# Performance work log

Measured on AMD Instinct MI355X. Metric: run time of the kernel, lower is better.

## Reference

```python
import jax, jax.numpy as jnp
import numpy as np
from jax import lax

# LNS semantics: values are held as (sign, log_base|x|); exact conversion round-trips
# make log-domain mul/add mathematically identical to float conv/linear/relu, so the
# faithful reference is the equivalent float pipeline.

def _conv(x, w, b):
    # x: [B,C,H,W], w: [O,C,kh,kw] (torch layout), stride 1, no padding
    y = lax.conv_general_dilated(x, w, window_strides=(1, 1), padding='VALID',
                                 dimension_numbers=('NCHW', 'OIHW', 'NCHW'))
    return y + b[None, :, None, None]

def _maxpool2(x):
    return lax.reduce_window(x, -jnp.inf, lax.max,
                             window_dimensions=(1, 1, 2, 2),
                             window_strides=(1, 1, 2, 2), padding='VALID')

def setup_inputs() -> dict:
    key = jax.random.key(0)
    ks = jax.random.split(key, 9)
    s = lambda k, shape, fan: jax.random.normal(k, shape, jnp.float32) * (1.0 / np.sqrt(fan))
    return {
        'x': jax.random.normal(ks[0], (512, 1, 54, 54), jnp.float32),
        'conv1_w': s(ks[1], (32, 1, 3, 3), 9),
        'conv1_b': s(ks[2], (32,), 9),
        'conv2_w': s(ks[3], (64, 32, 3, 3), 32 * 9),
        'conv2_b': s(ks[4], (64,), 32 * 9),
        'fc1_w': s(ks[5], (128, 9216), 9216),
        'fc1_b': s(ks[6], (128,), 9216),
        'fc2_w': s(ks[7], (10, 128), 128),
        'fc2_b': s(ks[8], (10,), 128),
    }

def reference(x, conv1_w, conv1_b, conv2_w, conv2_b, fc1_w, fc1_b, fc2_w, fc2_b):
    h = jnp.maximum(_conv(x, conv1_w, conv1_b), 0.0)          # [B,32,52,52]
    h = _maxpool2(h)                                          # [B,32,26,26]
    h = jnp.maximum(_conv(h, conv2_w, conv2_b), 0.0)          # [B,64,24,24]
    h = _maxpool2(h)                                          # [B,64,12,12]
    h = h.reshape(h.shape[0], -1)                             # [B,9216]
    h = jnp.maximum(h @ fc1_w.T + fc1_b, 0.0)                 # [B,128]
    return h @ fc2_w.T + fc2_b                                # [B,10]
```

## Files before the change

### kernel.cpp

```cpp
#include <hip/hip_runtime.h>


#define B 512
#define POS 676
#define ICP 36
#define P2SZ (64*12*12)

typedef unsigned short ushort_t;
typedef ushort_t ushort4v __attribute__((ext_vector_type(4)));
typedef short s16x8 __attribute__((ext_vector_type(8)));
typedef float f32x4 __attribute__((ext_vector_type(4)));
typedef float f32x2 __attribute__((ext_vector_type(2)));

__device__ __forceinline__ ushort_t f2bf(float f) {
    union { float f; unsigned u; } a; a.f = f;
    unsigned r = a.u + 0x7FFFu + ((a.u >> 16) & 1u);
    return (ushort_t)(r >> 16);
}
__device__ __forceinline__ float bf2f(ushort_t u) {
    union { unsigned u; float f; } a; a.u = ((unsigned)u) << 16;
    return a.f;
}

#define N_WR (64 * 9 * 32)
#define N_WF (128 * 9216)
#define CONV1_BLOCKS 1664
#define PREP_BLOCKS  4680

__global__ __launch_bounds__(256) void conv1_prep(const float* __restrict__ x,
                                                  const float* __restrict__ w,
                                                  const float* __restrict__ bias,
                                                  const float* __restrict__ c2w,
                                                  const float* __restrict__ f1w,
                                                  ushort_t* __restrict__ out,
                                                  ushort_t* __restrict__ wr,
                                                  ushort_t* __restrict__ wfb) {
    int blk = blockIdx.x;
    if (blk >= CONV1_BLOCKS) {
        int t = (blk - CONV1_BLOCKS) * 256 + threadIdx.x;
        if (t < N_WR) {
            int ic  = t & 31;
            int tap = (t >> 5) % 9;
            int oc  = t / 288;
            wr[t] = f2bf(c2w[oc * 288 + ic * 9 + tap]);
        } else if (t < N_WR + N_WF) {
            int i = t - N_WR;
            wfb[i] = f2bf(f1w[i]);
        }
        return;
    }
    int t = blk * 256 + threadIdx.x;
    int ic = t & 31;
    int r  = t >> 5;
    int py = r % 26;
    int b  = r / 26;

    const float* wp = w + ic * 9;
    float w00 = wp[0], w01 = wp[1], w02 = wp[2];
    float w10 = wp[3], w11 = wp[4], w12 = wp[5];
    float w20 = wp[6], w21 = wp[7], w22 = wp[8];
    float bv = bias[ic];

    const float* xr = x + b * (54 * 54) + (2 * py) * 54;
    ushort_t* po = out + ((size_t)b * POS + py * 26) * 32 + ic;

    f32x2 p[4], q[4];
#pragma unroll
    for (int rr = 0; rr < 4; ++rr) p[rr] = *reinterpret_cast<const f32x2*>(xr + rr * 54);
#pragma unroll
    for (int rr = 0; rr < 4; ++rr) q[rr] = *reinterpret_cast<const f32x2*>(xr + rr * 54 + 2);

#pragma unroll
    for (int px = 0; px < 26; ++px) {
        f32x2 mid[4];
#pragma unroll
        for (int rr = 0; rr < 4; ++rr) mid[rr] = (f32x2){p[rr].y, q[rr].x};

        f32x2 s0 = p[0] * (f32x2)w00 + mid[0] * (f32x2)w01 + q[0] * (f32x2)w02
                 + p[1] * (f32x2)w10 + mid[1] * (f32x2)w11 + q[1] * (f32x2)w12
                 + p[2] * (f32x2)w20 + mid[2] * (f32x2)w21 + q[2] * (f32x2)w22;
        f32x2 s1 = p[1] * (f32x2)w00 + mid[1] * (f32x2)w01 + q[1] * (f32x2)w02
                 + p[2] * (f32x2)w10 + mid[2] * (f32x2)w11 + q[2] * (f32x2)w12
                 + p[3] * (f32x2)w20 + mid[3] * (f32x2)w21 + q[3] * (f32x2)w22;

        float m = fmaxf(fmaxf(s0.x, s0.y), fmaxf(s1.x, s1.y));
        po[px * 32] = f2bf(fmaxf(m + bv, 0.0f));
        if (px < 25) {
#pragma unroll
            for (int rr = 0; rr < 4; ++rr) {
                p[rr] = q[rr];
                q[rr] = *reinterpret_cast<const f32x2*>(xr + rr * 54 + 2 * px + 4);
            }
        }
    }
}

__global__ __launch_bounds__(256) void conv2_mfma(const ushort_t* __restrict__ p1,
                                                  const ushort_t* __restrict__ wr,
                                                  const float* __restrict__ bias,
                                                  ushort_t* __restrict__ pool2) {
    __shared__ ushort_t lds[260 * ICP];
    int blk = blockIdx.x;
    int b = blk / 3, c = blk % 3;
    int tid = threadIdx.x;

    const ushort_t* src = p1 + ((size_t)b * POS + 8 * c * 26) * 32;
    for (int t = tid; t < 260 * 8; t += 256) {
        int pos = t >> 3, off = (t & 7) * 4;
        ushort4v v = *reinterpret_cast<const ushort4v*>(src + pos * 32 + off);
        *reinterpret_cast<ushort4v*>(&lds[pos * ICP + off]) = v;
    }
    __syncthreads();

    int lane = tid & 63, wid = tid >> 6;
    int quad = lane >> 4, lr = lane & 15;

    int ebase[3];
#pragma unroll
    for (int t = 0; t < 3; ++t) {
        int m  = t * 16 + lr;
        int yl = m / 24;
        int xx = m - yl * 24;
        ebase[t] = ((2 * wid + yl) * 26 + xx) * ICP + quad * 8;
    }

    f32x4 acc[3][4];
#pragma unroll
    for (int t = 0; t < 3; ++t)
#pragma unroll
        for (int n = 0; n < 4; ++n) acc[t][n] = (f32x4){0.f, 0.f, 0.f, 0.f};

    const ushort_t* wb = wr + (size_t)lr * 288 + quad * 8;

#pragma unroll
    for (int tap = 0; tap < 9; ++tap) {
        int ky = tap / 3, kx = tap % 3;
        int koff = (ky * 26 + kx) * ICP;
        s16x8 a[3];
#pragma unroll
        for (int t = 0; t < 3; ++t) {
            union { ushort4v s[2]; s16x8 v; } u;
            u.s[0] = *reinterpret_cast<const ushort4v*>(&lds[ebase[t] + koff]);
            u.s[1] = *reinterpret_cast<const ushort4v*>(&lds[ebase[t] + koff + 4]);
            a[t] = u.v;
        }
        s16x8 bf[4];
#pragma unroll
        for (int n = 0; n < 4; ++n)
            bf[n] = *reinterpret_cast<const s16x8*>(wb + n * 4608 + tap * 32);
#pragma unroll
        for (int t = 0; t < 3; ++t)
#pragma unroll
            for (int n = 0; n < 4; ++n)
                acc[t][n] = __builtin_amdgcn_mfma_f32_16x16x32_bf16(a[t], bf[n], acc[t][n], 0, 0, 0);
    }
    __syncthreads();

    ushort_t* scr = lds + wid * 1536;
#pragma unroll
    for (int t = 0; t < 3; ++t)
#pragma unroll
        for (int n = 0; n < 4; ++n) {
            int oc = n * 16 + lr;
            int i0 = t * 8 + quad * 2;
            float v0 = fmaxf(acc[t][n][0], acc[t][n][1]);
            float v1 = fmaxf(acc[t][n][2], acc[t][n][3]);
            union { ushort_t u2[2]; unsigned w; } pk;
            pk.u2[0] = f2bf(v0); pk.u2[1] = f2bf(v1);
            *reinterpret_cast<unsigned*>(&scr[oc * 24 + i0]) = pk.w;
        }
    int oc = lane;
    const ushort_t* row = scr + oc * 24;
    float bv = bias[oc];
    int py = c * 4 + wid;
    ushort_t outv[12];
#pragma unroll
    for (int px = 0; px < 12; ++px) {
        float r0 = bf2f(row[px]);
        float r1 = bf2f(row[px + 12]);
        outv[px] = f2bf(fmaxf(fmaxf(r0, r1) + bv, 0.0f));
    }
    ushort_t* po = pool2 + ((size_t)(b * 64 + oc) * 144 + py * 12);
#pragma unroll
    for (int q = 0; q < 3; ++q)
        *reinterpret_cast<ushort4v*>(po + q * 4) =
            (ushort4v){outv[q*4+0], outv[q*4+1], outv[q*4+2], outv[q*4+3]};
}

__global__ __launch_bounds__(256) void fc1_mfma(const ushort_t* __restrict__ A,
                                                 const ushort_t* __restrict__ W,
                                                 float* __restrict__ Cpart) {
    int tid = threadIdx.x;
    int lane = tid & 63, wid = tid >> 6;
    int lr = lane & 15, quad = lane >> 4;
    int w  = blockIdx.x * 4 + wid;
    int nt = w & 3;
    int ks = (w >> 2) & 31;
    int mt = w >> 7;

    int m0 = mt * 32;
    int n0 = nt * 32;
    int k0 = ks * 288 + quad * 8;
    const ushort_t* a0 = A + (size_t)(m0 + lr) * 9216 + k0;
    const ushort_t* a1 = a0 + (size_t)16 * 9216;
    const ushort_t* b0 = W + (size_t)(n0 + lr) * 9216 + k0;
    const ushort_t* b1 = b0 + (size_t)16 * 9216;

    f32x4 acc[2][2];
#pragma unroll
    for (int i = 0; i < 2; ++i)
#pragma unroll
        for (int j = 0; j < 2; ++j) acc[i][j] = (f32x4){0.f, 0.f, 0.f, 0.f};

#pragma unroll
    for (int kk = 0; kk < 9; ++kk) {
        s16x8 av0 = *reinterpret_cast<const s16x8*>(a0 + kk * 32);
        s16x8 av1 = *reinterpret_cast<const s16x8*>(a1 + kk * 32);
        s16x8 bv0 = *reinterpret_cast<const s16x8*>(b0 + kk * 32);
        s16x8 bv1 = *reinterpret_cast<const s16x8*>(b1 + kk * 32);
        acc[0][0] = __builtin_amdgcn_mfma_f32_16x16x32_bf16(av0, bv0, acc[0][0], 0, 0, 0);
        acc[0][1] = __builtin_amdgcn_mfma_f32_16x16x32_bf16(av0, bv1, acc[0][1], 0, 0, 0);
        acc[1][0] = __builtin_amdgcn_mfma_f32_16x16x32_bf16(av1, bv0, acc[1][0], 0, 0, 0);
        acc[1][1] = __builtin_amdgcn_mfma_f32_16x16x32_bf16(av1, bv1, acc[1][1], 0, 0, 0);
    }

    float* cp = Cpart + (size_t)ks * (512 * 128);
#pragma unroll
    for (int i = 0; i < 2; ++i) {
        int crow = m0 + i * 16 + quad * 4;
#pragma unroll
        for (int j = 0; j < 2; ++j) {
            int col = n0 + j * 16 + lr;
#pragma unroll
            for (int r = 0; r < 4; ++r)
                cp[(size_t)(crow + r) * 128 + col] = acc[i][j][r];
        }
    }
}

__global__ __launch_bounds__(128) void fc1fc2(const float* __restrict__ Cpart,
                                              const float* __restrict__ b1,
                                              const float* __restrict__ w2,
                                              const float* __restrict__ b2,
                                              float* __restrict__ out) {
    __shared__ float h[128];
    int b = blockIdx.x, k = threadIdx.x;
    float s = 0.f;
#pragma unroll
    for (int ks = 0; ks < 32; ++ks) s += Cpart[(size_t)ks * (512 * 128) + b * 128 + k];
    h[k] = fmaxf(s + b1[k], 0.0f);
    __syncthreads();
    if (k < 10) {
        const float* wp = w2 + k * 128;
        float acc = 0.f;
#pragma unroll 8
        for (int j = 0; j < 128; ++j) acc += h[j] * wp[j];
        out[b * 10 + k] = acc + b2[k];
    }
}

extern "C" void kernel_launch(void* const* d_in, const int* in_sizes, int n_in,
                              void* d_out, int out_size, void* d_ws, size_t ws_size,
                              hipStream_t stream) {
    const float* x       = (const float*)d_in[0];
    const float* conv1_w = (const float*)d_in[1];
    const float* conv1_b = (const float*)d_in[2];
    const float* conv2_w = (const float*)d_in[3];
    const float* conv2_b = (const float*)d_in[4];
    const float* fc1_w   = (const float*)d_in[5];
    const float* fc1_b   = (const float*)d_in[6];
    const float* fc2_w   = (const float*)d_in[7];
    const float* fc2_b   = (const float*)d_in[8];
    float* out = (float*)d_out;

    char* ws = (char*)d_ws;
    ushort_t* pool1 = (ushort_t*)ws;
    ws += (size_t)B * POS * 32 * sizeof(ushort_t);
    ushort_t* wr = (ushort_t*)ws;
    ws += N_WR * sizeof(ushort_t) + 128;
    ushort_t* wfb = (ushort_t*)ws;
    ws += N_WF * sizeof(ushort_t) + 128;
    ushort_t* pool2b = (ushort_t*)ws;
    ws += (size_t)B * P2SZ * sizeof(ushort_t) + 128;
    float* Cpart = (float*)ws;
    ws += (size_t)32 * 512 * 128 * sizeof(float) + 128;

    {
        conv1_prep<<<CONV1_BLOCKS + PREP_BLOCKS, 256, 0, stream>>>(
            x, conv1_w, conv1_b, conv2_w, fc1_w, pool1, wr, wfb);
    }
    {
        conv2_mfma<<<B * 3, 256, 0, stream>>>(pool1, wr, conv2_b, pool2b);
    }
    {
        fc1_mfma<<<512, 256, 0, stream>>>(pool2b, wfb, Cpart);
    }
    {
        fc1fc2<<<B, 128, 0, stream>>>(Cpart, fc1_b, fc2_w, fc2_b, out);
    }
}
```

Measured before the change: 131.3 us.

## Fuse conv2, fc1 and fc2 into one persistent kernel with grid barriers

Merges the conv2, fc1 split-K and fc1-reduce/fc2 kernels into a single launch of 768 blocks. Each block handles two conv2 chunks, then software grid barriers built on atomic counters separate the stages. The barrier counters are reset inside the conv1 prep kernel. This removes two kernel launch gaps and their tail effects. In exchange it relies on all 768 blocks being co-resident (256 CUs at 3 blocks each), otherwise it deadlocks, and it adds atomic spin-wait costs.

New measurement: 437.7 us. 233% more time.

```diff
diff --git a/kernel.cpp b/kernel.cpp
--- a/kernel.cpp
+++ b/kernel.cpp
@@ -26,6 +26,7 @@
 #define N_WF (128 * 9216)
 #define CONV1_BLOCKS 1664
 #define PREP_BLOCKS  4680
+#define FUSED_BLOCKS 768
 
 __global__ __launch_bounds__(256) void conv1_prep(const float* __restrict__ x,
                                                   const float* __restrict__ w,
@@ -34,9 +35,11 @@
                                                   const float* __restrict__ f1w,
                                                   ushort_t* __restrict__ out,
                                                   ushort_t* __restrict__ wr,
-                                                  ushort_t* __restrict__ wfb) {
+                                                  ushort_t* __restrict__ wfb,
+                                                  unsigned* __restrict__ barrier_ctr) {
     int blk = blockIdx.x;
     if (blk >= CONV1_BLOCKS) {
+        if (blk == CONV1_BLOCKS && threadIdx.x < 2) barrier_ctr[threadIdx.x] = 0;
         int t = (blk - CONV1_BLOCKS) * 256 + threadIdx.x;
         if (t < N_WR) {
             int ic  = t & 31;
@@ -95,167 +98,188 @@
     }
 }
 
-__global__ __launch_bounds__(256) void conv2_mfma(const ushort_t* __restrict__ p1,
-                                                  const ushort_t* __restrict__ wr,
-                                                  const float* __restrict__ bias,
-                                                  ushort_t* __restrict__ pool2) {
+__device__ __forceinline__ void grid_barrier(unsigned* ctr, unsigned target) {
+    __threadfence();
+    __syncthreads();
+    if (threadIdx.x == 0) {
+        atomicAdd(ctr, 1u);
+        while (__hip_atomic_load(ctr, __ATOMIC_RELAXED, __HIP_MEMORY_SCOPE_AGENT) < target)
+            __builtin_amdgcn_s_sleep(8);
+        __threadfence();
+    }
+    __syncthreads();
+}
+
+__global__ __launch_bounds__(256, 3) void fused_net(const ushort_t* __restrict__ p1,
+                                                    const ushort_t* __restrict__ wr,
+                                                    const float* __restrict__ c2b,
+                                                    const ushort_t* __restrict__ wfb,
+                                                    const float* __restrict__ b1,
+                                                    const float* __restrict__ w2,
+                                                    const float* __restrict__ b2,
+                                                    ushort_t* __restrict__ pool2,
+                                                    float* __restrict__ Cpart,
+                                                    float* __restrict__ out,
+                                                    unsigned* __restrict__ barrier_ctr) {
     __shared__ ushort_t lds[260 * ICP];
     int blk = blockIdx.x;
-    int b = blk / 3, c = blk % 3;
     int tid = threadIdx.x;
-
-    const ushort_t* src = p1 + ((size_t)b * POS + 8 * c * 26) * 32;
-    for (int t = tid; t < 260 * 8; t += 256) {
-        int pos = t >> 3, off = (t & 7) * 4;
-        ushort4v v = *reinterpret_cast<const ushort4v*>(src + pos * 32 + off);
-        *reinterpret_cast<ushort4v*>(&lds[pos * ICP + off]) = v;
-    }
-    __syncthreads();
-
     int lane = tid & 63, wid = tid >> 6;
     int quad = lane >> 4, lr = lane & 15;
 
-    int ebase[3];
-#pragma unroll
-    for (int t = 0; t < 3; ++t) {
-        int m  = t * 16 + lr;
-        int yl = m / 24;
-        int xx = m - yl * 24;
-        ebase[t] = ((2 * wid + yl) * 26 + xx) * ICP + quad * 8;
-    }
-
-    f32x4 acc[3][4];
-#pragma unroll
-    for (int t = 0; t < 3; ++t)
-#pragma unroll
-        for (int n = 0; n < 4; ++n) acc[t][n] = (f32x4){0.f, 0.f, 0.f, 0.f};
-
-    const ushort_t* wb = wr + (size_t)lr * 288 + quad * 8;
-
-#pragma unroll
-    for (int tap = 0; tap < 9; ++tap) {
-        int ky = tap / 3, kx = tap % 3;
-        int koff = (ky * 26 + kx) * ICP;
-        s16x8 a[3];
+#pragma unroll 1
+    for (int cc = 0; cc < 2; ++cc) {
+        int ch = blk * 2 + cc;
+        int b = ch / 3, c = ch % 3;
+
+        const ushort_t* src = p1 + ((size_t)b * POS + 8 * c * 26) * 32;
+        for (int t = tid; t < 260 * 8; t += 256) {
+            int pos = t >> 3, off = (t & 7) * 4;
+            ushort4v v = *reinterpret_cast<const ushort4v*>(src + pos * 32 + off);
+            *reinterpret_cast<ushort4v*>(&lds[pos * ICP + off]) = v;
+        }
+        __syncthreads();
+
+        int ebase[3];
 #pragma unroll
         for (int t = 0; t < 3; ++t) {
-            union { ushort4v s[2]; s16x8 v; } u;
-            u.s[0] = *reinterpret_cast<const ushort4v*>(&lds[ebase[t] + koff]);
-            u.s[1] = *reinterpret_cast<const ushort4v*>(&lds[ebase[t] + koff + 4]);
-            a[t] = u.v;
-        }
-        s16x8 bf[4];
-#pragma unroll
-        for (int n = 0; n < 4; ++n)
-            bf[n] = *reinterpret_cast<const s16x8*>(wb + n * 4608 + tap * 32);
+            int m  = t * 16 + lr;
+            int yl = m / 24;
+            int xx = m - yl * 24;
+            ebase[t] = ((2 * wid + yl) * 26 + xx) * ICP + quad * 8;
+        }
+
+        f32x4 acc[3][4];
 #pragma unroll
         for (int t = 0; t < 3; ++t)
 #pragma unroll
+            for (int n = 0; n < 4; ++n) acc[t][n] = (f32x4){0.f, 0.f, 0.f, 0.f};
+
+        const ushort_t* wb = wr + (size_t)lr * 288 + quad * 8;
+
+#pragma unroll
+        for (int tap = 0; tap < 9; ++tap) {
+            int ky = tap / 3, kx = tap % 3;
+            int koff = (ky * 26 + kx) * ICP;
+            s16x8 a[3];
+#pragma unroll
+            for (int t = 0; t < 3; ++t) {
+                union { ushort4v s[2]; s16x8 v; } u;
+                u.s[0] = *reinterpret_cast<const ushort4v*>(&lds[ebase[t] + koff]);
+                u.s[1] = *reinterpret_cast<const ushort4v*>(&lds[ebase[t] + koff + 4]);
+                a[t] = u.v;
+            }
+            s16x8 bf[4];
+#pragma unroll
             for (int n = 0; n < 4; ++n)
-                acc[t][n] = __builtin_amdgcn_mfma_f32_16x16x32_bf16(a[t], bf[n], acc[t][n], 0, 0, 0);
-    }
-    __syncthreads();
-
-    ushort_t* scr = lds + wid * 1536;
-#pragma unroll
-    for (int t = 0; t < 3; ++t)
-#pragma unroll
-        for (int n = 0; n < 4; ++n) {
-            int oc = n * 16 + lr;
-            int i0 = t * 8 + quad * 2;
-            float v0 = fmaxf(acc[t][n][0], acc[t][n][1]);
-            float v1 = fmaxf(acc[t][n][2], acc[t][n][3]);
-            union { ushort_t u2[2]; unsigned w; } pk;
-            pk.u2[0] = f2bf(v0); pk.u2[1] = f2bf(v1);
-            *reinterpret_cast<unsigned*>(&scr[oc * 24 + i0]) = pk.w;
-        }
-    int oc = lane;
-    const ushort_t* row = scr + oc * 24;
-    float bv = bias[oc];
-    int py = c * 4 + wid;
-    ushort_t outv[12];
-#pragma unroll
-    for (int px = 0; px < 12; ++px) {
-        float r0 = bf2f(row[px]);
-        float r1 = bf2f(row[px + 12]);
-        outv[px] = f2bf(fmaxf(fmaxf(r0, r1) + bv, 0.0f));
-    }
-    ushort_t* po = pool2 + ((size_t)(b * 64 + oc) * 144 + py * 12);
-#pragma unroll
-    for (int q = 0; q < 3; ++q)
-        *reinterpret_cast<ushort4v*>(po + q * 4) =
-            (ushort4v){outv[q*4+0], outv[q*4+1], outv[q*4+2], outv[q*4+3]};
-}
-
-__global__ __launch_bounds__(256) void fc1_mfma(const ushort_t* __restrict__ A,
-                                                 const ushort_t* __restrict__ W,
-                                                 float* __restrict__ Cpart) {
-    int tid = threadIdx.x;
-    int lane = tid & 63, wid = tid >> 6;
-    int lr = lane & 15, quad = lane >> 4;
-    int w  = blockIdx.x * 4 + wid;
-    int nt = w & 3;
-    int ks = (w >> 2) & 31;
-    int mt = w >> 7;
-
-    int m0 = mt * 32;
-    int n0 = nt * 32;
-    int k0 = ks * 288 + quad * 8;
-    const ushort_t* a0 = A + (size_t)(m0 + lr) * 9216 + k0;
-    const ushort_t* a1 = a0 + (size_t)16 * 9216;
-    const ushort_t* b0 = W + (size_t)(n0 + lr) * 9216 + k0;
-    const ushort_t* b1 = b0 + (size_t)16 * 9216;
-
-    f32x4 acc[2][2];
-#pragma unroll
-    for (int i = 0; i < 2; ++i)
-#pragma unroll
-        for (int j = 0; j < 2; ++j) acc[i][j] = (f32x4){0.f, 0.f, 0.f, 0.f};
-
-#pragma unroll
-    for (int kk = 0; kk < 9; ++kk) {
-        s16x8 av0 = *reinterpret_cast<const s16x8*>(a0 + kk * 32);
-        s16x8 av1 = *reinterpret_cast<const s16x8*>(a1 + kk * 32);
-        s16x8 bv0 = *reinterpret_cast<const s16x8*>(b0 + kk * 32);
-        s16x8 bv1 = *reinterpret_cast<const s16x8*>(b1 + kk * 32);
-        acc[0][0] = __builtin_amdgcn_mfma_f32_16x16x32_bf16(av0, bv0, acc[0][0], 0, 0, 0);
-        acc[0][1] = __builtin_amdgcn_mfma_f32_16x16x32_bf16(av0, bv1, acc[0][1], 0, 0, 0);
-        acc[1][0] = __builtin_amdgcn_mfma_f32_16x16x32_bf16(av1, bv0, acc[1][0], 0, 0, 0);
-        acc[1][1] = __builtin_amdgcn_mfma_f32_16x16x32_bf16(av1, bv1, acc[1][1], 0, 0, 0);
-    }
-
-    float* cp = Cpart + (size_t)ks * (512 * 128);
-#pragma unroll
-    for (int i = 0; i < 2; ++i) {
-        int crow = m0 + i * 16 + quad * 4;
-#pragma unroll
-        for (int j = 0; j < 2; ++j) {
-            int col = n0 + j * 16 + lr;
-#pragma unroll
-            for (int r = 0; r < 4; ++r)
-                cp[(size_t)(crow + r) * 128 + col] = acc[i][j][r];
-        }
-    }
-}
-
-__global__ __launch_bounds__(128) void fc1fc2(const float* __restrict__ Cpart,
-                                              const float* __restrict__ b1,
-                                              const float* __restrict__ w2,
-                                              const float* __restrict__ b2,
-                                              float* __restrict__ out) {
-    __shared__ float h[128];
-    int b = blockIdx.x, k = threadIdx.x;
-    float s = 0.f;
-#pragma unroll
-    for (int ks = 0; ks < 32; ++ks) s += Cpart[(size_t)ks * (512 * 128) + b * 128 + k];
-    h[k] = fmaxf(s + b1[k], 0.0f);
-    __syncthreads();
-    if (k < 10) {
-        const float* wp = w2 + k * 128;
-        float acc = 0.f;
+                bf[n] = *reinterpret_cast<const s16x8*>(wb + n * 4608 + tap * 32);
+#pragma unroll
+            for (int t = 0; t < 3; ++t)
+#pragma unroll
+                for (int n = 0; n < 4; ++n)
+                    acc[t][n] = __builtin_amdgcn_mfma_f32_16x16x32_bf16(a[t], bf[n], acc[t][n], 0, 0, 0);
+        }
+        __syncthreads();
+
+        ushort_t* scr = lds + wid * 1536;
+#pragma unroll
+        for (int t = 0; t < 3; ++t)
+#pragma unroll
+            for (int n = 0; n < 4; ++n) {
+                int oc = n * 16 + lr;
+                int i0 = t * 8 + quad * 2;
+                float v0 = fmaxf(acc[t][n][0], acc[t][n][1]);
+                float v1 = fmaxf(acc[t][n][2], acc[t][n][3]);
+                union { ushort_t u2[2]; unsigned w; } pk;
+                pk.u2[0] = f2bf(v0); pk.u2[1] = f2bf(v1);
+                *reinterpret_cast<unsigned*>(&scr[oc * 24 + i0]) = pk.w;
+            }
+        int oc = lane;
+        const ushort_t* row = scr + oc * 24;
+        float bv = c2b[oc];
+        int py = c * 4 + wid;
+        ushort_t outv[12];
+#pragma unroll
+        for (int px = 0; px < 12; ++px) {
+            float r0 = bf2f(row[px]);
+            float r1 = bf2f(row[px + 12]);
+            outv[px] = f2bf(fmaxf(fmaxf(r0, r1) + bv, 0.0f));
+        }
+        ushort_t* po = pool2 + ((size_t)(b * 64 + oc) * 144 + py * 12);
+#pragma unroll
+        for (int q = 0; q < 3; ++q)
+            *reinterpret_cast<ushort4v*>(po + q * 4) =
+                (ushort4v){outv[q*4+0], outv[q*4+1], outv[q*4+2], outv[q*4+3]};
+        __syncthreads();
+    }
+
+    grid_barrier(&barrier_ctr[0], FUSED_BLOCKS);
+
+    if (blk < 512) {
+        int job = blk * 4 + wid;
+        int nt = job & 3;
+        int ks = (job >> 2) & 31;
+        int mt = job >> 7;
+
+        int m0 = mt * 32;
+        int n0 = nt * 32;
+        int k0 = ks * 288 + quad * 8;
+        const ushort_t* a0 = pool2 + (size_t)(m0 + lr) * 9216 + k0;
+        const ushort_t* a1 = a0 + (size_t)16 * 9216;
+        const ushort_t* b0 = wfb + (size_t)(n0 + lr) * 9216 + k0;
+        const ushort_t* bq1 = b0 + (size_t)16 * 9216;
+
+        f32x4 facc[2][2];
+#pragma unroll
+        for (int i = 0; i < 2; ++i)
+#pragma unroll
+            for (int j = 0; j < 2; ++j) facc[i][j] = (f32x4){0.f, 0.f, 0.f, 0.f};
+
+#pragma unroll
+        for (int kk = 0; kk < 9; ++kk) {
+            s16x8 av0 = *reinterpret_cast<const s16x8*>(a0 + kk * 32);
+            s16x8 av1 = *reinterpret_cast<const s16x8*>(a1 + kk * 32);
+            s16x8 bv0 = *reinterpret_cast<const s16x8*>(b0 + kk * 32);
+            s16x8 bv1 = *reinterpret_cast<const s16x8*>(bq1 + kk * 32);
+            facc[0][0] = __builtin_amdgcn_mfma_f32_16x16x32_bf16(av0, bv0, facc[0][0], 0, 0, 0);
+            facc[0][1] = __builtin_amdgcn_mfma_f32_16x16x32_bf16(av0, bv1, facc[0][1], 0, 0, 0);
+            facc[1][0] = __builtin_amdgcn_mfma_f32_16x16x32_bf16(av1, bv0, facc[1][0], 0, 0, 0);
+            facc[1][1] = __builtin_amdgcn_mfma_f32_16x16x32_bf16(av1, bv1, facc[1][1], 0, 0, 0);
+        }
+
+        float* cp = Cpart + (size_t)ks * (512 * 128);
+#pragma unroll
+        for (int i = 0; i < 2; ++i) {
+            int crow = m0 + i * 16 + quad * 4;
+#pragma unroll
+            for (int j = 0; j < 2; ++j) {
+                int col = n0 + j * 16 + lr;
+#pragma unroll
+                for (int r = 0; r < 4; ++r)
+                    cp[(size_t)(crow + r) * 128 + col] = facc[i][j][r];
+            }
+        }
+    }
+
+    grid_barrier(&barrier_ctr[1], FUSED_BLOCKS);
+
+    if (blk < 512) {
+        float* hsh = reinterpret_cast<float*>(lds);
+        int b = blk, k = tid;
+        if (k < 128) {
+            float s = 0.f;
+#pragma unroll
+            for (int ks = 0; ks < 32; ++ks) s += Cpart[(size_t)ks * (512 * 128) + b * 128 + k];
+            hsh[k] = fmaxf(s + b1[k], 0.0f);
+        }
+        __syncthreads();
+        if (k < 10) {
+            const float* wp = w2 + k * 128;
+            float acc = 0.f;
 #pragma unroll 8
-        for (int j = 0; j < 128; ++j) acc += h[j] * wp[j];
-        out[b * 10 + k] = acc + b2[k];
+            for (int j = 0; j < 128; ++j) acc += hsh[j] * wp[j];
+            out[b * 10 + k] = acc + b2[k];
+        }
     }
 }
 
@@ -284,18 +308,15 @@
     ws += (size_t)B * P2SZ * sizeof(ushort_t) + 128;
     float* Cpart = (float*)ws;
     ws += (size_t)32 * 512 * 128 * sizeof(float) + 128;
+    unsigned* barrier_ctr = (unsigned*)ws;
+    ws += 256;
 
     {
         conv1_prep<<<CONV1_BLOCKS + PREP_BLOCKS, 256, 0, stream>>>(
-            x, conv1_w, conv1_b, conv2_w, fc1_w, pool1, wr, wfb);
+            x, conv1_w, conv1_b, conv2_w, fc1_w, pool1, wr, wfb, barrier_ctr);
     }
     {
-        conv2_mfma<<<B * 3, 256, 0, stream>>>(pool1, wr, conv2_b, pool2b);
-    }
-    {
-        fc1_mfma<<<512, 256, 0, stream>>>(pool2b, wfb, Cpart);
-    }
-    {
-        fc1fc2<<<B, 128, 0, stream>>>(Cpart, fc1_b, fc2_w, fc2_b, out);
-    }
-}
+        fused_net<<<FUSED_BLOCKS, 256, 0, stream>>>(
+            pool1, wr, conv2_b, wfb, fc1_b, fc2_w, fc2_b, pool2b, Cpart, out, barrier_ctr);
+    }
+}
```

## Store pool2 channels-last with permuted fc1 weights and split conv1 rows

Applied to the files above, without the earlier changes.

Conv2 now writes its pooled output channels-last ([b][pos][oc]), and the fc1 weight conversion permutes columns to match, so the flatten order stays consistent. Conv1 work is split so each thread handles half a pooled row, doubling block count for more parallelism. Per-lane conv2 stores become contiguous across lanes (64 oc adjacent) instead of strided per-channel vectors, trading vectorized 8-byte stores for coalesced 2-byte stores. The weight permutation uses strided gathers from fc1_w, which may slow the prep step.

Result: no change. 131.2 us (-0.1%).

```diff
diff --git a/kernel.cpp b/kernel.cpp
--- a/kernel.cpp
+++ b/kernel.cpp
@@ -24,7 +24,7 @@
 
 #define N_WR (64 * 9 * 32)
 #define N_WF (128 * 9216)
-#define CONV1_BLOCKS 1664
+#define CONV1_BLOCKS 3328
 #define PREP_BLOCKS  4680
 
 __global__ __launch_bounds__(256) void conv1_prep(const float* __restrict__ x,
@@ -44,16 +44,22 @@
             int oc  = t / 288;
             wr[t] = f2bf(c2w[oc * 288 + ic * 9 + tap]);
         } else if (t < N_WR + N_WF) {
-            int i = t - N_WR;
-            wfb[i] = f2bf(f1w[i]);
+            int i  = t - N_WR;
+            int oc  = i & 63;
+            int pos = (i >> 6) % 144;
+            int n   = i / 9216;
+            wfb[i] = f2bf(f1w[(size_t)n * 9216 + oc * 144 + pos]);
         }
         return;
     }
     int t = blk * 256 + threadIdx.x;
     int ic = t & 31;
     int r  = t >> 5;
-    int py = r % 26;
-    int b  = r / 26;
+    int h  = r & 1;
+    int r2 = r >> 1;
+    int py = r2 % 26;
+    int b  = r2 / 26;
+    int px0 = h * 13;
 
     const float* wp = w + ic * 9;
     float w00 = wp[0], w01 = wp[1], w02 = wp[2];
@@ -61,8 +67,8 @@
     float w20 = wp[6], w21 = wp[7], w22 = wp[8];
     float bv = bias[ic];
 
-    const float* xr = x + b * (54 * 54) + (2 * py) * 54;
-    ushort_t* po = out + ((size_t)b * POS + py * 26) * 32 + ic;
+    const float* xr = x + b * (54 * 54) + (2 * py) * 54 + 2 * px0;
+    ushort_t* po = out + ((size_t)b * POS + py * 26 + px0) * 32 + ic;
 
     f32x2 p[4], q[4];
 #pragma unroll
@@ -71,7 +77,7 @@
     for (int rr = 0; rr < 4; ++rr) q[rr] = *reinterpret_cast<const f32x2*>(xr + rr * 54 + 2);
 
 #pragma unroll
-    for (int px = 0; px < 26; ++px) {
+    for (int j = 0; j < 13; ++j) {
         f32x2 mid[4];
 #pragma unroll
         for (int rr = 0; rr < 4; ++rr) mid[rr] = (f32x2){p[rr].y, q[rr].x};
@@ -84,12 +90,12 @@
                  + p[3] * (f32x2)w20 + mid[3] * (f32x2)w21 + q[3] * (f32x2)w22;
 
         float m = fmaxf(fmaxf(s0.x, s0.y), fmaxf(s1.x, s1.y));
-        po[px * 32] = f2bf(fmaxf(m + bv, 0.0f));
-        if (px < 25) {
+        po[j * 32] = f2bf(fmaxf(m + bv, 0.0f));
+        if (j < 12) {
 #pragma unroll
             for (int rr = 0; rr < 4; ++rr) {
                 p[rr] = q[rr];
-                q[rr] = *reinterpret_cast<const f32x2*>(xr + rr * 54 + 2 * px + 4);
+                q[rr] = *reinterpret_cast<const f32x2*>(xr + rr * 54 + 2 * j + 4);
             }
         }
     }
@@ -98,7 +104,7 @@
 __global__ __launch_bounds__(256) void conv2_mfma(const ushort_t* __restrict__ p1,
                                                   const ushort_t* __restrict__ wr,
                                                   const float* __restrict__ bias,
-                                                  ushort_t* __restrict__ pool2) {
+                                                  ushort_t* __restrict__ pool2cl) {
     __shared__ ushort_t lds[260 * ICP];
     int blk = blockIdx.x;
     int b = blk / 3, c = blk % 3;
@@ -173,18 +179,13 @@
     const ushort_t* row = scr + oc * 24;
     float bv = bias[oc];
     int py = c * 4 + wid;
-    ushort_t outv[12];
+    ushort_t* po = pool2cl + ((size_t)b * 144 + py * 12) * 64 + oc;
 #pragma unroll
     for (int px = 0; px < 12; ++px) {
         float r0 = bf2f(row[px]);
         float r1 = bf2f(row[px + 12]);
-        outv[px] = f2bf(fmaxf(fmaxf(r0, r1) + bv, 0.0f));
-    }
-    ushort_t* po = pool2 + ((size_t)(b * 64 + oc) * 144 + py * 12);
-#pragma unroll
-    for (int q = 0; q < 3; ++q)
-        *reinterpret_cast<ushort4v*>(po + q * 4) =
-            (ushort4v){outv[q*4+0], outv[q*4+1], outv[q*4+2], outv[q*4+3]};
+        po[px * 64] = f2bf(fmaxf(fmaxf(r0, r1) + bv, 0.0f));
+    }
 }
 
 __global__ __launch_bounds__(256) void fc1_mfma(const ushort_t* __restrict__ A,
@@ -280,7 +281,7 @@
     ws += N_WR * sizeof(ushort_t) + 128;
     ushort_t* wfb = (ushort_t*)ws;
     ws += N_WF * sizeof(ushort_t) + 128;
-    ushort_t* pool2b = (ushort_t*)ws;
+    ushort_t* pool2cl = (ushort_t*)ws;
     ws += (size_t)B * P2SZ * sizeof(ushort_t) + 128;
     float* Cpart = (float*)ws;
     ws += (size_t)32 * 512 * 128 * sizeof(float) + 128;
@@ -290,10 +291,10 @@
             x, conv1_w, conv1_b, conv2_w, fc1_w, pool1, wr, wfb);
     }
     {
-        conv2_mfma<<<B * 3, 256, 0, stream>>>(pool1, wr, conv2_b, pool2b);
+        conv2_mfma<<<B * 3, 256, 0, stream>>>(pool1, wr, conv2_b, pool2cl);
     }
     {
-        fc1_mfma<<<512, 256, 0, stream>>>(pool2b, wfb, Cpart);
+        fc1_mfma<<<512, 256, 0, stream>>>(pool2cl, wfb, Cpart);
     }
     {
         fc1fc2<<<B, 128, 0, stream>>>(Cpart, fc1_b, fc2_w, fc2_b, out);
```
